# Kernel tuning notes

Hardware: AMD Instinct MI355X
Metric: run time of the kernel (lower is better)

The kernel has to match this reference:

```python
import jax, jax.numpy as jnp
import numpy as np

N_NODES = 100000
N_EDGES = 1600000
D_IN = 128
D_HID = 128


def gcn_conv(x, src, dst, W, b, n_nodes):
    """PyG-style GCNConv: out = D^{-1/2} (A + I) D^{-1/2} (x @ W) + b.

    src/dst already include self-loops.
    """
    deg = jax.ops.segment_sum(jnp.ones_like(src, dtype=x.dtype), dst,
                              num_segments=n_nodes)
    dinv = jnp.where(deg > 0, deg ** -0.5, 0.0)
    norm = dinv[src] * dinv[dst]              # [E]
    h = x @ W                                  # [N, d_out]
    msg = h[src] * norm[:, None]               # gather + scale, [E, d_out]
    out = jax.ops.segment_sum(msg, dst, num_segments=n_nodes)
    return out + b


def setup_inputs() -> dict:
    key = jax.random.key(0)
    k1, k2, k3, k4 = jax.random.split(key, 4)
    x = jax.random.normal(k1, (N_NODES, D_IN), dtype=jnp.float32)
    edge_index = jax.random.randint(k2, (2, N_EDGES), 0, N_NODES, dtype=jnp.int64)
    s1 = (1.0 / np.sqrt(D_IN)).astype(np.float32)
    s2 = (1.0 / np.sqrt(D_HID)).astype(np.float32)
    W1 = jax.random.normal(k3, (D_IN, D_HID), dtype=jnp.float32) * s1
    b1 = jnp.zeros((D_HID,), dtype=jnp.float32)
    W2 = jax.random.normal(k4, (D_HID, D_HID), dtype=jnp.float32) * s2
    b2 = jnp.zeros((D_HID,), dtype=jnp.float32)
    return {"x": x, "edge_index": edge_index, "W1": W1, "b1": b1,
            "W2": W2, "b2": b2}


def reference(x, edge_index, W1, b1, W2, b2):
    n_nodes = x.shape[0]
    loops = jnp.arange(n_nodes, dtype=edge_index.dtype)
    src = jnp.concatenate([edge_index[0], loops])  # self-loops, as PyG default
    dst = jnp.concatenate([edge_index[1], loops])
    h = gcn_conv(x, src, dst, W1, b1, n_nodes)
    h = gcn_conv(h, src, dst, W2, b2, n_nodes)
    return h
```

## Files before the change

### kernel.cpp

```cpp
#include <hip/hip_runtime.h>

#define N_NODES 100000
#define N_EDGES 1600000

#define NBIN 196
#define BINCAP 9216
#define NPB 4096
#define EPT 16
#define BPT 36
#define PBLK ((N_EDGES + NPB - 1) / NPB)
#define GG ((N_NODES + 63) / 64)

typedef unsigned int uint;
typedef unsigned short u16;
typedef unsigned long long u64;
typedef __attribute__((ext_vector_type(8))) short bf16x8;
typedef __attribute__((ext_vector_type(4))) float f32x4;

__device__ __forceinline__ uint bf16_rtne(float f) {
  uint u = __float_as_uint(f);
  return (u + 0x7fffu + ((u >> 16) & 1u)) >> 16;
}


__global__ __launch_bounds__(256) void k_prep(const float* __restrict__ W1, const float* __restrict__ W2,
                                              const float* __restrict__ b1,
                                              uint* __restrict__ S12, float* __restrict__ bW2,
                                              int* __restrict__ bin_cur) {
  int u = blockIdx.x * 256 + threadIdx.x;
  int lane = u & 63;
  int kcnt = u >> 6;
  int kc = kcnt & 3;
  int nt = kcnt >> 2;
  int n = nt * 16 + (lane & 15);
  int k0 = kc * 32 + (lane >> 4) * 8;
  float f[8];
#pragma unroll
  for (int j = 0; j < 8; ++j) f[j] = 0.f;
  for (int m = 0; m < 128; ++m) {
    float w2v = W2[(size_t)m * 128 + n];
#pragma unroll
    for (int j = 0; j < 8; ++j) f[j] += W1[(size_t)(k0 + j) * 128 + m] * w2v;
  }
  uint4 pk;
  pk.x = bf16_rtne(f[0]) | (bf16_rtne(f[1]) << 16);
  pk.y = bf16_rtne(f[2]) | (bf16_rtne(f[3]) << 16);
  pk.z = bf16_rtne(f[4]) | (bf16_rtne(f[5]) << 16);
  pk.w = bf16_rtne(f[6]) | (bf16_rtne(f[7]) << 16);
  ((uint4*)S12)[u] = pk;
  if (blockIdx.x == 0) {
    if (threadIdx.x < NBIN) bin_cur[threadIdx.x] = 0;
    if (threadIdx.x < 128) {
      int c = threadIdx.x;
      float acc = 0.f;
      for (int m = 0; m < 128; ++m) acc += b1[m] * W2[(size_t)m * 128 + c];
      bW2[c] = acc;
    }
  }
}


__device__ __forceinline__ void part_body(int bid, const int* __restrict__ ei,
                                          int* __restrict__ bin_cur, uint* __restrict__ stage,
                                          uint* smem) {
  uint* hist  = smem;
  uint* wbase = smem + 4 * NBIN;
  uint* lcur  = smem + 8 * NBIN;
  const int t = threadIdx.x;
  const int w = t >> 6;
  const int e0 = bid * NPB;
  for (int i = t; i < 4 * NBIN; i += 256) { hist[i] = 0; lcur[i] = 0; }
  __syncthreads();
  uint d[EPT];
#pragma unroll
  for (int j = 0; j < EPT; ++j) {
    int e = e0 + j * 256 + t;
    d[j] = (e < N_EDGES) ? (uint)ei[N_EDGES + e] : 0xFFFFFFFFu;
    if (d[j] != 0xFFFFFFFFu) atomicAdd(&hist[w * NBIN + (d[j] >> 9)], 1u);
  }
  __syncthreads();
  if (t < NBIN) {
    uint h0 = hist[t], h1 = hist[NBIN + t], h2 = hist[2 * NBIN + t], h3 = hist[3 * NBIN + t];
    uint tot = h0 + h1 + h2 + h3;
    uint g = tot ? (uint)atomicAdd(&bin_cur[t], (int)tot) : 0u;
    wbase[t] = g;
    wbase[NBIN + t] = g + h0;
    wbase[2 * NBIN + t] = g + h0 + h1;
    wbase[3 * NBIN + t] = g + h0 + h1 + h2;
  }
  __syncthreads();
#pragma unroll
  for (int j = 0; j < EPT; ++j) {
    if (d[j] != 0xFFFFFFFFu) {
      int e = e0 + j * 256 + t;
      uint s = (uint)ei[e];
      uint b = d[j] >> 9;
      uint pos = wbase[w * NBIN + b] + atomicAdd(&lcur[w * NBIN + b], 1u);
      if (pos < BINCAP)
        stage[(size_t)b * BINCAP + pos] = s | ((d[j] & 511u) << 17);
    }
  }
}

__device__ __forceinline__ void gemm_body(int gb, const float* __restrict__ x,
                                          const uint* __restrict__ Wsw, u16* __restrict__ OutH,
                                          uint* smem) {
  uint* As = smem;
  uint* Bs = smem + 4096;
  const int tid = threadIdx.x;
  const int R = gb * 64;
  {
    const uint4* src = (const uint4*)Wsw;
    uint4* dst = (uint4*)Bs;
#pragma unroll
    for (int v = 0; v < 8; ++v) dst[tid + v * 256] = src[tid + v * 256];
  }
  const int unit = tid & 15;
  const int kc_s = unit >> 2;
  const int quad_s = unit & 3;
#pragma unroll
  for (int pass = 0; pass < 4; ++pass) {
    int row = pass * 16 + (tid >> 4);
    int gr = R + row;
    if (gr >= N_NODES) gr = N_NODES - 1;
    const float* srcr = x + (size_t)gr * 128 + unit * 8;
    float4 f0 = ((const float4*)srcr)[0];
    float4 f1 = ((const float4*)srcr)[1];
    uint4 pk;
    pk.x = bf16_rtne(f0.x) | (bf16_rtne(f0.y) << 16);
    pk.y = bf16_rtne(f0.z) | (bf16_rtne(f0.w) << 16);
    pk.z = bf16_rtne(f1.x) | (bf16_rtne(f1.y) << 16);
    pk.w = bf16_rtne(f1.z) | (bf16_rtne(f1.w) << 16);
    int lane_t = quad_s * 16 + (row & 15);
    *(uint4*)&As[((pass * 4 + kc_s) * 64 + lane_t) * 4] = pk;
  }
  __syncthreads();

  const int w = tid >> 6;
  const int lane = tid & 63;
  bf16x8 a0 = *(bf16x8*)&As[((w * 4 + 0) * 64 + lane) * 4];
  bf16x8 a1 = *(bf16x8*)&As[((w * 4 + 1) * 64 + lane) * 4];
  bf16x8 a2 = *(bf16x8*)&As[((w * 4 + 2) * 64 + lane) * 4];
  bf16x8 a3 = *(bf16x8*)&As[((w * 4 + 3) * 64 + lane) * 4];
  f32x4 acc[8];
#pragma unroll
  for (int nt = 0; nt < 8; ++nt) acc[nt] = (f32x4){0.f, 0.f, 0.f, 0.f};
#pragma unroll
  for (int nt = 0; nt < 8; ++nt) {
    bf16x8 b0 = *(bf16x8*)&Bs[((nt * 4 + 0) * 64 + lane) * 4];
    bf16x8 b1 = *(bf16x8*)&Bs[((nt * 4 + 1) * 64 + lane) * 4];
    bf16x8 b2 = *(bf16x8*)&Bs[((nt * 4 + 2) * 64 + lane) * 4];
    bf16x8 b3 = *(bf16x8*)&Bs[((nt * 4 + 3) * 64 + lane) * 4];
    acc[nt] = __builtin_amdgcn_mfma_f32_16x16x32_bf16(a0, b0, acc[nt], 0, 0, 0);
    acc[nt] = __builtin_amdgcn_mfma_f32_16x16x32_bf16(a1, b1, acc[nt], 0, 0, 0);
    acc[nt] = __builtin_amdgcn_mfma_f32_16x16x32_bf16(a2, b2, acc[nt], 0, 0, 0);
    acc[nt] = __builtin_amdgcn_mfma_f32_16x16x32_bf16(a3, b3, acc[nt], 0, 0, 0);
  }
  const int colb = lane & 15;
  const int quad = lane >> 4;
#pragma unroll
  for (int nt = 0; nt < 8; ++nt) {
#pragma unroll
    for (int r = 0; r < 4; ++r) {
      int gr = R + w * 16 + quad * 4 + r;
      if (gr < N_NODES)
        OutH[(size_t)gr * 128 + nt * 16 + colb] = (u16)bf16_rtne(acc[nt][r]);
    }
  }
}

__global__ __launch_bounds__(256) void k_pg(const int* __restrict__ ei, int* __restrict__ bin_cur,
                                            uint* __restrict__ stage,
                                            const float* __restrict__ x, const uint* __restrict__ Wsw,
                                            u16* __restrict__ OutH) {
  __shared__ uint smem[12288];
  if ((int)blockIdx.x < PBLK) part_body(blockIdx.x, ei, bin_cur, stage, smem);
  else                        gemm_body(blockIdx.x - PBLK, x, Wsw, OutH, smem);
}


__global__ __launch_bounds__(256) void k_bin2(const int* __restrict__ bin_cur, const uint* __restrict__ stage,
                                              float* __restrict__ dinv, int* __restrict__ rowptr,
                                              int* __restrict__ ep) {
  __shared__ int cnt[512];
  __shared__ int sd[256];
  __shared__ int curs[512];
  const int b = blockIdx.x, t = threadIdx.x;
  int vg = (t < NBIN) ? min(bin_cur[t], BINCAP) : 0;
  sd[t] = vg;
  __syncthreads();
  for (int off = 1; off < 256; off <<= 1) {
    int a = (t >= off) ? sd[t - off] : 0;
    __syncthreads();
    sd[t] += a;
    __syncthreads();
  }
  const int eb = (b > 0) ? sd[b - 1] : 0;
  if (b == 0 && t == 0) rowptr[N_NODES] = sd[NBIN - 1];
  __syncthreads();

  cnt[t] = 0; cnt[t + 256] = 0;
  __syncthreads();
  const int n = min(bin_cur[b], BINCAP);
  const uint* sb = stage + (size_t)b * BINCAP;
  uint r[BPT];
#pragma unroll
  for (int j = 0; j < BPT; ++j) {
    int i = j * 256 + t;
    r[j] = (i < n) ? sb[i] : 0xFFFFFFFFu;
  }
#pragma unroll
  for (int j = 0; j < BPT; ++j)
    if (r[j] != 0xFFFFFFFFu) atomicAdd(&cnt[r[j] >> 17], 1);
  __syncthreads();
  int v0 = cnt[t * 2], v1 = cnt[t * 2 + 1];
  int s = v0 + v1;
  sd[t] = s;
  __syncthreads();
  for (int off = 1; off < 256; off <<= 1) {
    int a = (t >= off) ? sd[t - off] : 0;
    __syncthreads();
    sd[t] += a;
    __syncthreads();
  }
  int run = sd[t] - s;
  int c0 = eb + run, c1 = eb + run + v0;
  int g0 = b * 512 + t * 2;
  if (g0 < N_NODES) {
    rowptr[g0] = c0;
    dinv[g0] = rsqrtf((float)(v0 + 1));
  }
  if (g0 + 1 < N_NODES) {
    rowptr[g0 + 1] = c1;
    dinv[g0 + 1] = rsqrtf((float)(v1 + 1));
  }
  curs[t * 2] = c0; curs[t * 2 + 1] = c1;
  __syncthreads();
#pragma unroll
  for (int j = 0; j < BPT; ++j)
    if (r[j] != 0xFFFFFFFFu) {
      int pos = atomicAdd(&curs[r[j] >> 17], 1);
      ep[pos] = (int)(r[j] & 0x1FFFFu);
    }
}


__device__ __forceinline__ void bacc(float& ax, float& ay, uint v, float w) {
  ax += w * __uint_as_float(v << 16);
  ay += w * __uint_as_float(v & 0xffff0000u);
}

__device__ __forceinline__ void agg_node(const uint* __restrict__ hb, const float* __restrict__ dinv,
                                         const int* __restrict__ ep, int node, int lane,
                                         int beg, int end, float dn, float& ax, float& ay, float& sw) {
  uint selfv = hb[(size_t)node * 64 + lane];
  bacc(ax, ay, selfv, dn);
  int e = beg;
  for (; e + 8 <= end; e += 8) {
    int p[8];
#pragma unroll
    for (int j = 0; j < 8; ++j) p[j] = ep[e + j];
    float wt[8];
#pragma unroll
    for (int j = 0; j < 8; ++j) wt[j] = dinv[p[j]];
    uint v[8];
#pragma unroll
    for (int j = 0; j < 8; ++j) v[j] = hb[(size_t)p[j] * 64 + lane];
#pragma unroll
    for (int j = 0; j < 8; ++j) { bacc(ax, ay, v[j], wt[j]); sw += wt[j]; }
  }
  if (e + 4 <= end) {
    int p[4];
#pragma unroll
    for (int j = 0; j < 4; ++j) p[j] = ep[e + j];
    float wt[4];
#pragma unroll
    for (int j = 0; j < 4; ++j) wt[j] = dinv[p[j]];
    uint v[4];
#pragma unroll
    for (int j = 0; j < 4; ++j) v[j] = hb[(size_t)p[j] * 64 + lane];
#pragma unroll
    for (int j = 0; j < 4; ++j) { bacc(ax, ay, v[j], wt[j]); sw += wt[j]; }
    e += 4;
  }
  for (; e < end; ++e) {
    int p = ep[e];
    float wt = dinv[p];
    uint v = hb[(size_t)p * 64 + lane];
    bacc(ax, ay, v, wt);
    sw += wt;
  }
}


__global__ __launch_bounds__(256) void k_agg1(const uint* __restrict__ hb, const float* __restrict__ dinv,
                                              const int* __restrict__ rowptr, const int* __restrict__ ep,
                                              u16* __restrict__ outb, float* __restrict__ sArr) {
  int wid = threadIdx.x >> 6;
  int lane = threadIdx.x & 63;
  int node = blockIdx.x * 4 + wid;
  if (node >= N_NODES) return;
  int beg = rowptr[node];
  int end = rowptr[node + 1];
  float dn = dinv[node];
  float ax = 0.f, ay = 0.f, sw = 0.f;
  agg_node(hb, dinv, ep, node, lane, beg, end, dn, ax, ay, sw);
  int c = lane * 2;
  uint pk = bf16_rtne(dn * ax) | (bf16_rtne(dn * ay) << 16);
  *(uint*)(outb + (size_t)node * 128 + c) = pk;
  if (lane == 0) sArr[node] = dn * (dn + sw);
}


__global__ __launch_bounds__(256) void k_agg2(const uint* __restrict__ hb, const float* __restrict__ dinv,
                                              const int* __restrict__ rowptr, const int* __restrict__ ep,
                                              const float* __restrict__ sArr, const float* __restrict__ bW2,
                                              const float* __restrict__ b2,
                                              float* __restrict__ outf) {
  int wid = threadIdx.x >> 6;
  int lane = threadIdx.x & 63;
  int node = blockIdx.x * 4 + wid;
  if (node >= N_NODES) return;
  int beg = rowptr[node];
  int end = rowptr[node + 1];
  float dn = dinv[node];
  float ax = 0.f, ay = 0.f, sw = 0.f;
  agg_node(hb, dinv, ep, node, lane, beg, end, dn, ax, ay, sw);
  float si = sArr[node];
  int c = lane * 2;
  float2 o;
  o.x = dn * ax + si * bW2[c] + b2[c];
  o.y = dn * ay + si * bW2[c + 1] + b2[c + 1];
  *(float2*)(outf + (size_t)node * 128 + c) = o;
}


extern "C" void kernel_launch(void* const* d_in, const int* in_sizes, int n_in,
                              void* d_out, int out_size, void* d_ws, size_t ws_size,
                              hipStream_t stream) {
  const float* x  = (const float*)d_in[0];
  const int*   ei = (const int*)d_in[1];
  const float* W1 = (const float*)d_in[2];
  const float* b1 = (const float*)d_in[3];
  const float* W2 = (const float*)d_in[4];
  const float* b2 = (const float*)d_in[5];
  float* out = (float*)d_out;

  char* p = (char*)d_ws;
  uint*  hb     = (uint*)p;  p += (size_t)N_NODES * 64 * sizeof(uint);
  int*   ep     = (int*)p;   p += (size_t)N_EDGES * sizeof(int);
  uint*  wsw1   = (uint*)p;  p += 8192 * sizeof(uint);
  float* bW2    = (float*)p; p += 128 * sizeof(float);
  float* dinv   = (float*)p; p += (size_t)N_NODES * sizeof(float);
  int*   rowptr = (int*)p;   p += (size_t)(N_NODES + 1) * sizeof(int);
  float* sArr   = (float*)p; p += (size_t)N_NODES * sizeof(float);
  int*   bin_cur= (int*)p;   p += (size_t)NBIN * sizeof(int);
  p = (char*)(((uintptr_t)p + 255) & ~(uintptr_t)255);
  uint*  stage  = (uint*)p;
  u16*   h1b    = (u16*)p;

  k_prep<<<8, 256, 0, stream>>>(W1, W2, b1, wsw1, bW2, bin_cur);
  k_pg<<<PBLK + GG, 256, 0, stream>>>(ei, bin_cur, stage, x, wsw1, (u16*)hb);
  k_bin2<<<NBIN, 256, 0, stream>>>(bin_cur, stage, dinv, rowptr, ep);
  k_agg1<<<(N_NODES + 3) / 4, 256, 0, stream>>>(hb, dinv, rowptr, ep, h1b, sArr);
  k_agg2<<<(N_NODES + 3) / 4, 256, 0, stream>>>((const uint*)h1b, dinv, rowptr, ep, sArr, bW2, b2, out);
}
```

Baseline: 294.5 us.

## Use finer destination bins and read GEMM weights directly from global

Raises the bin count from 196 bins of 512 destinations to 782 bins of 128 destinations, with smaller capacity and per-thread load count. The partition kernel now keeps two per-wave histograms instead of four, and the bin kernel scans four bin counts per thread. The GEMM path stops staging the weight matrix in shared memory and loads B fragments straight from global or cache. Together this cuts shared memory per block and gives k_bin2 more, smaller blocks for better occupancy. The trade-off is more global atomics on bin cursors and a higher chance a bin overflows its smaller capacity.

```diff
diff --git a/kernel.cpp b/kernel.cpp
--- a/kernel.cpp
+++ b/kernel.cpp
@@ -3,11 +3,11 @@
 #define N_NODES 100000
 #define N_EDGES 1600000
 
-#define NBIN 196
-#define BINCAP 9216
+#define NBIN 782
+#define BINCAP 2560
 #define NPB 4096
 #define EPT 16
-#define BPT 36
+#define BPT 10
 #define PBLK ((N_EDGES + NPB - 1) / NPB)
 #define GG ((N_NODES + 63) / 64)
 
@@ -49,7 +49,7 @@
   pk.w = bf16_rtne(f[6]) | (bf16_rtne(f[7]) << 16);
   ((uint4*)S12)[u] = pk;
   if (blockIdx.x == 0) {
-    if (threadIdx.x < NBIN) bin_cur[threadIdx.x] = 0;
+    for (int i = threadIdx.x; i < NBIN; i += 256) bin_cur[i] = 0;
     if (threadIdx.x < 128) {
       int c = threadIdx.x;
       float acc = 0.f;
@@ -64,29 +64,27 @@
                                           int* __restrict__ bin_cur, uint* __restrict__ stage,
                                           uint* smem) {
   uint* hist  = smem;
-  uint* wbase = smem + 4 * NBIN;
-  uint* lcur  = smem + 8 * NBIN;
+  uint* wbase = smem + 2 * NBIN;
+  uint* lcur  = smem + 4 * NBIN;
   const int t = threadIdx.x;
-  const int w = t >> 6;
+  const int w = (t >> 6) & 1;
   const int e0 = bid * NPB;
-  for (int i = t; i < 4 * NBIN; i += 256) { hist[i] = 0; lcur[i] = 0; }
+  for (int i = t; i < 2 * NBIN; i += 256) { hist[i] = 0; lcur[i] = 0; }
   __syncthreads();
   uint d[EPT];
 #pragma unroll
   for (int j = 0; j < EPT; ++j) {
     int e = e0 + j * 256 + t;
     d[j] = (e < N_EDGES) ? (uint)ei[N_EDGES + e] : 0xFFFFFFFFu;
-    if (d[j] != 0xFFFFFFFFu) atomicAdd(&hist[w * NBIN + (d[j] >> 9)], 1u);
-  }
-  __syncthreads();
-  if (t < NBIN) {
-    uint h0 = hist[t], h1 = hist[NBIN + t], h2 = hist[2 * NBIN + t], h3 = hist[3 * NBIN + t];
-    uint tot = h0 + h1 + h2 + h3;
-    uint g = tot ? (uint)atomicAdd(&bin_cur[t], (int)tot) : 0u;
-    wbase[t] = g;
-    wbase[NBIN + t] = g + h0;
-    wbase[2 * NBIN + t] = g + h0 + h1;
-    wbase[3 * NBIN + t] = g + h0 + h1 + h2;
+    if (d[j] != 0xFFFFFFFFu) atomicAdd(&hist[w * NBIN + (d[j] >> 7)], 1u);
+  }
+  __syncthreads();
+  for (int i = t; i < NBIN; i += 256) {
+    uint h0 = hist[i], h1 = hist[NBIN + i];
+    uint tot = h0 + h1;
+    uint g = tot ? (uint)atomicAdd(&bin_cur[i], (int)tot) : 0u;
+    wbase[i] = g;
+    wbase[NBIN + i] = g + h0;
   }
   __syncthreads();
 #pragma unroll
@@ -94,27 +92,19 @@
     if (d[j] != 0xFFFFFFFFu) {
       int e = e0 + j * 256 + t;
       uint s = (uint)ei[e];
-      uint b = d[j] >> 9;
+      uint b = d[j] >> 7;
       uint pos = wbase[w * NBIN + b] + atomicAdd(&lcur[w * NBIN + b], 1u);
       if (pos < BINCAP)
-        stage[(size_t)b * BINCAP + pos] = s | ((d[j] & 511u) << 17);
+        stage[(size_t)b * BINCAP + pos] = s | ((d[j] & 127u) << 17);
     }
   }
 }
 
 __device__ __forceinline__ void gemm_body(int gb, const float* __restrict__ x,
                                           const uint* __restrict__ Wsw, u16* __restrict__ OutH,
-                                          uint* smem) {
-  uint* As = smem;
-  uint* Bs = smem + 4096;
+                                          uint* As) {
   const int tid = threadIdx.x;
   const int R = gb * 64;
-  {
-    const uint4* src = (const uint4*)Wsw;
-    uint4* dst = (uint4*)Bs;
-#pragma unroll
-    for (int v = 0; v < 8; ++v) dst[tid + v * 256] = src[tid + v * 256];
-  }
   const int unit = tid & 15;
   const int kc_s = unit >> 2;
   const int quad_s = unit & 3;
@@ -147,10 +137,10 @@
   for (int nt = 0; nt < 8; ++nt) acc[nt] = (f32x4){0.f, 0.f, 0.f, 0.f};
 #pragma unroll
   for (int nt = 0; nt < 8; ++nt) {
-    bf16x8 b0 = *(bf16x8*)&Bs[((nt * 4 + 0) * 64 + lane) * 4];
-    bf16x8 b1 = *(bf16x8*)&Bs[((nt * 4 + 1) * 64 + lane) * 4];
-    bf16x8 b2 = *(bf16x8*)&Bs[((nt * 4 + 2) * 64 + lane) * 4];
-    bf16x8 b3 = *(bf16x8*)&Bs[((nt * 4 + 3) * 64 + lane) * 4];
+    bf16x8 b0 = *(const bf16x8*)((const uint4*)Wsw + (nt * 4 + 0) * 64 + lane);
+    bf16x8 b1 = *(const bf16x8*)((const uint4*)Wsw + (nt * 4 + 1) * 64 + lane);
+    bf16x8 b2 = *(const bf16x8*)((const uint4*)Wsw + (nt * 4 + 2) * 64 + lane);
+    bf16x8 b3 = *(const bf16x8*)((const uint4*)Wsw + (nt * 4 + 3) * 64 + lane);
     acc[nt] = __builtin_amdgcn_mfma_f32_16x16x32_bf16(a0, b0, acc[nt], 0, 0, 0);
     acc[nt] = __builtin_amdgcn_mfma_f32_16x16x32_bf16(a1, b1, acc[nt], 0, 0, 0);
     acc[nt] = __builtin_amdgcn_mfma_f32_16x16x32_bf16(a2, b2, acc[nt], 0, 0, 0);
@@ -173,7 +163,7 @@
                                             uint* __restrict__ stage,
                                             const float* __restrict__ x, const uint* __restrict__ Wsw,
                                             u16* __restrict__ OutH) {
-  __shared__ uint smem[12288];
+  __shared__ uint smem[4736];
   if ((int)blockIdx.x < PBLK) part_body(blockIdx.x, ei, bin_cur, stage, smem);
   else                        gemm_body(blockIdx.x - PBLK, x, Wsw, OutH, smem);
 }
@@ -182,12 +172,20 @@
 __global__ __launch_bounds__(256) void k_bin2(const int* __restrict__ bin_cur, const uint* __restrict__ stage,
                                               float* __restrict__ dinv, int* __restrict__ rowptr,
                                               int* __restrict__ ep) {
-  __shared__ int cnt[512];
   __shared__ int sd[256];
-  __shared__ int curs[512];
+  __shared__ int cnt[128];
+  __shared__ int curs[128];
+  __shared__ int ebs;
   const int b = blockIdx.x, t = threadIdx.x;
-  int vg = (t < NBIN) ? min(bin_cur[t], BINCAP) : 0;
-  sd[t] = vg;
+  int v[4];
+  int s = 0;
+#pragma unroll
+  for (int j = 0; j < 4; ++j) {
+    int i = t * 4 + j;
+    v[j] = (i < NBIN) ? min(bin_cur[i], BINCAP) : 0;
+    s += v[j];
+  }
+  sd[t] = s;
   __syncthreads();
   for (int off = 1; off < 256; off <<= 1) {
     int a = (t >= off) ? sd[t - off] : 0;
@@ -195,12 +193,18 @@
     sd[t] += a;
     __syncthreads();
   }
-  const int eb = (b > 0) ? sd[b - 1] : 0;
-  if (b == 0 && t == 0) rowptr[N_NODES] = sd[NBIN - 1];
-  __syncthreads();
-
-  cnt[t] = 0; cnt[t + 256] = 0;
-  __syncthreads();
+  int run = sd[t] - s;
+#pragma unroll
+  for (int j = 0; j < 4; ++j) {
+    int i = t * 4 + j;
+    if (i == b) ebs = run;
+    run += v[j];
+  }
+  if (b == 0 && t == 255) rowptr[N_NODES] = sd[255];
+  if (t < 128) cnt[t] = 0;
+  __syncthreads();
+  const int eb = ebs;
+
   const int n = min(bin_cur[b], BINCAP);
   const uint* sb = stage + (size_t)b * BINCAP;
   uint r[BPT];
@@ -213,9 +217,8 @@
   for (int j = 0; j < BPT; ++j)
     if (r[j] != 0xFFFFFFFFu) atomicAdd(&cnt[r[j] >> 17], 1);
   __syncthreads();
-  int v0 = cnt[t * 2], v1 = cnt[t * 2 + 1];
-  int s = v0 + v1;
-  sd[t] = s;
+  int v0 = (t < 128) ? cnt[t] : 0;
+  sd[t] = v0;
   __syncthreads();
   for (int off = 1; off < 256; off <<= 1) {
     int a = (t >= off) ? sd[t - off] : 0;
@@ -223,18 +226,16 @@
     sd[t] += a;
     __syncthreads();
   }
-  int run = sd[t] - s;
-  int c0 = eb + run, c1 = eb + run + v0;
-  int g0 = b * 512 + t * 2;
-  if (g0 < N_NODES) {
-    rowptr[g0] = c0;
-    dinv[g0] = rsqrtf((float)(v0 + 1));
-  }
-  if (g0 + 1 < N_NODES) {
-    rowptr[g0 + 1] = c1;
-    dinv[g0 + 1] = rsqrtf((float)(v1 + 1));
-  }
-  curs[t * 2] = c0; curs[t * 2 + 1] = c1;
+  int run2 = sd[t] - v0;
+  if (t < 128) {
+    int g = b * 128 + t;
+    int c0 = eb + run2;
+    if (g < N_NODES) {
+      rowptr[g] = c0;
+      dinv[g] = rsqrtf((float)(v0 + 1));
+    }
+    curs[t] = c0;
+  }
   __syncthreads();
 #pragma unroll
   for (int j = 0; j < BPT; ++j)
```

Result: slower. 310.4 us (+5.4%).
